# Kernel tuning notes

Measured on AMD Instinct MI355X. Metric: run time of the kernel, lower is better.

The kernel has to match this reference:

```python
import jax, jax.numpy as jnp
import numpy as np

D_MODEL = 2048
NUM_HEADS = 16
KV_HEADS = 4
HEAD_DIM = D_MODEL // NUM_HEADS  # 128
SEQ = 4096
BATCH = 1
ROPE_THETA = 10000.0


def _rope_cache(T, dim, base, dtype):
    inv_freq = 1.0 / (base ** (jnp.arange(0, dim, 2, dtype=jnp.float32) / dim))
    t = jnp.arange(T, dtype=jnp.float32)
    freqs = jnp.outer(t, inv_freq)                      # (T, dim/2)
    emb = jnp.concatenate([freqs, freqs], axis=-1)      # (T, dim)
    return jnp.cos(emb).astype(dtype), jnp.sin(emb).astype(dtype)


def _rotate_half(x):
    d = x.shape[-1] // 2
    return jnp.concatenate([-x[..., d:], x[..., :d]], axis=-1)


def _apply_rope(q, k, cos, sin):
    # q: (B,T,Hq,D), k: (B,T,Hkv,D); cos/sin: (T,D) broadcast over heads
    c = cos[None, :, None, :]
    s = sin[None, :, None, :]
    q = q * c + _rotate_half(q) * s
    k = k * c + _rotate_half(k) * s
    return q, k


def setup_inputs() -> dict:
    key = jax.random.key(0)
    ks = jax.random.split(key, 6)
    sc = 1.0 / np.sqrt(D_MODEL)
    kv_out = KV_HEADS * HEAD_DIM
    return {
        "x": jax.random.normal(ks[0], (BATCH, SEQ, D_MODEL), dtype=jnp.float32),
        "Wq": jax.random.normal(ks[1], (D_MODEL, D_MODEL), dtype=jnp.float32) * sc,
        "Wk": jax.random.normal(ks[2], (D_MODEL, kv_out), dtype=jnp.float32) * sc,
        "Wv": jax.random.normal(ks[3], (D_MODEL, kv_out), dtype=jnp.float32) * sc,
        "Wo": jax.random.normal(ks[4], (D_MODEL, D_MODEL), dtype=jnp.float32) * sc,
        "bo": jax.random.normal(ks[5], (D_MODEL,), dtype=jnp.float32) * 0.01,
    }


def reference(x, Wq, Wk, Wv, Wo, bo):
    B, T, _ = x.shape
    q = (x @ Wq).reshape(B, T, NUM_HEADS, HEAD_DIM)
    k = (x @ Wk).reshape(B, T, KV_HEADS, HEAD_DIM)
    v = (x @ Wv).reshape(B, T, KV_HEADS, HEAD_DIM)

    cos, sin = _rope_cache(T, HEAD_DIM, ROPE_THETA, x.dtype)
    q, k = _apply_rope(q, k, cos, sin)

    reps = NUM_HEADS // KV_HEADS
    k = jnp.repeat(k, reps, axis=2)  # repeat_interleave on head dim
    v = jnp.repeat(v, reps, axis=2)

    # (B,H,T,D)
    q = q.transpose(0, 2, 1, 3)
    k = k.transpose(0, 2, 1, 3)
    v = v.transpose(0, 2, 1, 3)

    scores = jnp.einsum("bhqd,bhkd->bhqk", q, k)
    causal = jnp.triu(jnp.ones((T, T), dtype=bool), k=1)
    scores = jnp.where(causal[None, None], -jnp.inf, scores)
    attn = jax.nn.softmax(scores / jnp.sqrt(jnp.asarray(HEAD_DIM, x.dtype)), axis=-1)

    ctx = jnp.einsum("bhqk,bhkd->bhqd", attn, v)
    ctx = ctx.transpose(0, 2, 1, 3).reshape(B, T, D_MODEL)
    return ctx @ Wo + bo
```

## Files before the change

### kernel.cpp

```cpp
#include <hip/hip_runtime.h>
#include <cstdint>
#include <cstddef>

#define SEQ 4096
#define DM  2048
#define NH  16
#define KVH 4
#define HD  128
#define QSCALE (0.08838834764831845f * 1.4426950408889634f)

typedef short bf16_t;
typedef __attribute__((ext_vector_type(8))) short bf16x8;
typedef __attribute__((ext_vector_type(4))) float f32x4;
typedef __attribute__((ext_vector_type(4))) unsigned uint32x4;

__device__ __forceinline__ bf16_t f2b(float f) {
  unsigned u = __builtin_bit_cast(unsigned, f);
  u += 0x7fffu + ((u >> 16) & 1u);
  return (bf16_t)(u >> 16);
}
__device__ __forceinline__ float b2f(bf16_t s) {
  unsigned u = ((unsigned)(unsigned short)s) << 16;
  return __builtin_bit_cast(float, u);
}
__device__ __forceinline__ unsigned cvtpk(float lo, float hi) {
  unsigned r;
  asm("v_cvt_pk_bf16_f32 %0, %1, %2" : "=v"(r) : "v"(lo), "v"(hi));
  return r;
}

__device__ __forceinline__ void gload_lds16(const void* gsrc, void* ldst) {
  __builtin_amdgcn_global_load_lds(
      (__attribute__((address_space(1))) void*)gsrc,
      (__attribute__((address_space(3))) void*)ldst, 16, 0, 0);
}

__global__ void cast_x_bf16(const float* __restrict__ x, bf16_t* __restrict__ xb, int n4) {
  int i = blockIdx.x * 256 + threadIdx.x;
  if (i >= n4) return;
  float4 v = ((const float4*)x)[i];
  union { bf16_t h[4]; unsigned long long u; } o;
  o.h[0] = f2b(v.x); o.h[1] = f2b(v.y); o.h[2] = f2b(v.z); o.h[3] = f2b(v.w);
  ((unsigned long long*)xb)[i] = o.u;
}

__global__ void transpose_cast_w(const float* __restrict__ W, bf16_t* __restrict__ Wt,
                                 int K, int N) {
  __shared__ float tile[32][33];
  int k0 = blockIdx.y * 32, n0 = blockIdx.x * 32;
  int tx = threadIdx.x, ty = threadIdx.y;
#pragma unroll
  for (int dy = 0; dy < 32; dy += 8)
    tile[ty + dy][tx] = W[(size_t)(k0 + ty + dy) * N + n0 + tx];
  __syncthreads();
#pragma unroll
  for (int dy = 0; dy < 32; dy += 8)
    Wt[(size_t)(n0 + ty + dy) * K + k0 + tx] = f2b(tile[tx][ty + dy]);
}

__global__ void rope_tab(float* __restrict__ ct, float* __restrict__ st) {
  int i = blockIdx.x * 256 + threadIdx.x;
  if (i >= SEQ * 64) return;
  int t = i >> 6, j = i & 63;
  float invf = expf(-(float)j * (9.210340371976184f / 64.0f));
  float ang = (float)t * invf;
  ct[i] = cosf(ang);
  st[i] = sinf(ang);
}

__global__ void rope_apply(bf16_t* __restrict__ Qb, bf16_t* __restrict__ KVb,
                           const float* __restrict__ ct, const float* __restrict__ st) {
  int i = blockIdx.x * 256 + threadIdx.x;
  const int qtot = SEQ * NH * 64;
  const int tot = qtot + SEQ * KVH * 64;
  if (i >= tot) return;
  bf16_t* base; int t, j; float scl;
  if (i < qtot) {
    t = i >> 10; int rem = i & 1023; int hh = rem >> 6; j = rem & 63;
    base = Qb + (size_t)t * DM + hh * HD;
    scl = QSCALE;
  } else {
    int i2 = i - qtot;
    t = i2 >> 8; int rem = i2 & 255; int hh = rem >> 6; j = rem & 63;
    base = KVb + (size_t)t * 1024 + hh * HD;
    scl = 1.0f;
  }
  float c = ct[t * 64 + j], s = st[t * 64 + j];
  float x0 = b2f(base[j]);
  float x1 = b2f(base[j + 64]);
  base[j]      = f2b((x0 * c - x1 * s) * scl);
  base[j + 64] = f2b((x1 * c + x0 * s) * scl);
}

__global__ void transpose_v(const bf16_t* __restrict__ KVb, bf16_t* __restrict__ Vt) {
  __shared__ bf16_t tile[32][33];
  int t0 = blockIdx.y * 32, d0 = blockIdx.x * 32;
  int tx = threadIdx.x, ty = threadIdx.y;
#pragma unroll
  for (int dy = 0; dy < 32; dy += 8)
    tile[ty + dy][tx] = KVb[(size_t)(t0 + ty + dy) * 1024 + 512 + d0 + tx];
  __syncthreads();
  int tt = t0 + tx;
  int j = (tt & ~63) | (tt & 32) | ((tt & 12) << 1) | ((tt & 16) >> 2) | (tt & 3);
#pragma unroll
  for (int dy = 0; dy < 32; dy += 8)
    Vt[(size_t)(d0 + ty + dy) * SEQ + j] = tile[tx][ty + dy];
}

template <int MODE>
__global__ __launch_bounds__(256, MODE == 0 ? 3 : 2)
void gemm_bt(const bf16_t* __restrict__ A, const bf16_t* __restrict__ Bt,
             void* __restrict__ C0out, void* __restrict__ C1out,
             const float* __restrict__ bias, int M, int N, int K) {
  __shared__ __align__(16) bf16_t ldsA[128 * 64];
  __shared__ __align__(16) bf16_t ldsB[128 * 64];
  const int t = threadIdx.x;
  const int w = t >> 6, l = t & 63;
  const int lg = l >> 4, lr = l & 15;
  const int bm = blockIdx.y, bn = blockIdx.x;
  const int wr = (w >> 1) * 64, wc = (w & 1) * 64;

  f32x4 acc[4][4] = {};

  for (int k0 = 0; k0 < K; k0 += 64) {
    __syncthreads();
#pragma unroll
    for (int i = 0; i < 4; ++i) {
      int idx = i * 256 + t;
      int row = idx >> 3;
      int ch  = (idx & 7) ^ (row & 7);
      gload_lds16(A  + (size_t)(bm * 128 + row) * K + k0 + ch * 8, &ldsA[idx * 8]);
      gload_lds16(Bt + (size_t)(bn * 128 + row) * K + k0 + ch * 8, &ldsB[idx * 8]);
    }
    __syncthreads();
#pragma unroll
    for (int kk = 0; kk < 2; ++kk) {
      bf16x8 af[4], bfr[4];
#pragma unroll
      for (int m = 0; m < 4; ++m) {
        int row = wr + m * 16 + lr;
        int ch = (kk * 4 + lg) ^ (row & 7);
        af[m] = *(const bf16x8*)&ldsA[row * 64 + ch * 8];
      }
#pragma unroll
      for (int n = 0; n < 4; ++n) {
        int row = wc + n * 16 + lr;
        int ch = (kk * 4 + lg) ^ (row & 7);
        bfr[n] = *(const bf16x8*)&ldsB[row * 64 + ch * 8];
      }
#pragma unroll
      for (int m = 0; m < 4; ++m)
#pragma unroll
        for (int n = 0; n < 4; ++n)
          acc[m][n] = __builtin_amdgcn_mfma_f32_16x16x32_bf16(af[m], bfr[n], acc[m][n], 0, 0, 0);
    }
  }

  const int row0 = bm * 128 + wr + lg * 4;
  if (MODE == 1) {
    float* C = (float*)C0out;
    const int col0 = bn * 128 + wc + lr;
#pragma unroll
    for (int n = 0; n < 4; ++n) {
      int col = col0 + n * 16;
      float b = bias[col];
#pragma unroll
      for (int m = 0; m < 4; ++m)
#pragma unroll
        for (int r = 0; r < 4; ++r)
          C[(size_t)(row0 + m * 16 + r) * N + col] = acc[m][n][r] + b;
    }
  } else {
    const int colbase = bn * 128 + wc;
    bf16_t* C; int stride, cb;
    if (colbase < 2048) { C = (bf16_t*)C0out; stride = 2048; cb = colbase; }
    else                { C = (bf16_t*)C1out; stride = 1024; cb = colbase - 2048; }
#pragma unroll
    for (int m = 0; m < 4; ++m)
#pragma unroll
      for (int n = 0; n < 4; ++n) {
        int col = cb + n * 16 + lr;
#pragma unroll
        for (int r = 0; r < 4; ++r)
          C[(size_t)(row0 + m * 16 + r) * stride + col] = f2b(acc[m][n][r]);
      }
  }
}

__global__ __launch_bounds__(512, 4)
void attn_fwd(const bf16_t* __restrict__ Qb, const bf16_t* __restrict__ KVb,
              const bf16_t* __restrict__ Vt, bf16_t* __restrict__ ctx) {
  __shared__ __align__(16) bf16_t kt[2][64 * 128];
  __shared__ __align__(16) bf16_t vts[2][128 * 64];

  const int t = threadIdx.x;
  const int w = t >> 6, l = t & 63;
  const int lg = l >> 4, lr = l & 15;
  const int h = blockIdx.y, g = h >> 2;
  const int b = blockIdx.x;
  const int m = w >> 2, wq = w & 3;
  const int qt = m ? 63 - b : b;
  const int qrow0 = qt * 64 + wq * 16;

  bf16x8 qf[4];
#pragma unroll
  for (int kk = 0; kk < 4; ++kk)
    qf[kk] = *(const bf16x8*)&Qb[(size_t)(qrow0 + lr) * DM + h * HD + kk * 32 + lg * 8];

  f32x4 acc[9] = {};
  float m_run = -1e30f;

  bf16x8 ones;
#pragma unroll
  for (int i = 0; i < 8; ++i) ones[i] = (short)0x3F80;

  const bf16_t* ksrc = KVb + g * 128;
  const bf16_t* vsrc = Vt + (size_t)(g * 128) * SEQ;
  auto stage = [&](int buf, int kvt) {
#pragma unroll
    for (int i = 0; i < 2; ++i) {
      int idx = i * 512 + t;
      int row = idx >> 4;
      int ch = (idx & 15) ^ (row & 7);
      gload_lds16(ksrc + (size_t)(kvt * 64 + row) * 1024 + ch * 8, &kt[buf][idx * 8]);
    }
#pragma unroll
    for (int i = 0; i < 2; ++i) {
      int idx = i * 512 + t;
      int row = idx >> 3;
      int ch = (idx & 7) ^ (row & 7);
      gload_lds16(vsrc + (size_t)row * SEQ + kvt * 64 + ch * 8, &vts[buf][idx * 8]);
    }
  };

  const int nkv = 64 - b;
  stage(0, 0);

  for (int kv = 0; kv < nkv; ++kv) {
    const int cur = kv & 1;
    const int kv0 = kv * 64;
    __syncthreads();
    if (kv + 1 < nkv) stage(cur ^ 1, kv + 1);

    if (kv <= qt) {
      f32x4 s[4] = {};
      __builtin_amdgcn_s_setprio(1);
#pragma unroll
      for (int n = 0; n < 4; ++n) {
        int row = n * 16 + lr;
#pragma unroll
        for (int kk = 0; kk < 4; ++kk) {
          int ch = (kk * 4 + lg) ^ (row & 7);
          bf16x8 kf = *(const bf16x8*)&kt[cur][row * 128 + ch * 8];
          s[n] = __builtin_amdgcn_mfma_f32_16x16x32_bf16(kf, qf[kk], s[n], 0, 0, 0);
        }
      }
      __builtin_amdgcn_s_setprio(0);

      const int qrow = qrow0 + lr;
      if (kv == qt) {
#pragma unroll
        for (int n = 0; n < 4; ++n)
#pragma unroll
          for (int r = 0; r < 4; ++r) {
            int key = kv0 + n * 16 + lg * 4 + r;
            if (key > qrow) s[n][r] = -1e30f;
          }
      }

      float pm = s[0][0];
#pragma unroll
      for (int n = 0; n < 4; ++n)
#pragma unroll
        for (int r = 0; r < 4; ++r)
          pm = fmaxf(pm, s[n][r]);
      pm = fmaxf(pm, __shfl_xor(pm, 16, 64));
      pm = fmaxf(pm, __shfl_xor(pm, 32, 64));

      if (__any((int)(pm > m_run + 8.f))) {
        float mn = fmaxf(m_run, pm);
        float a_s = exp2f(m_run - mn);
        m_run = mn;
        float alpha[4];
#pragma unroll
        for (int r = 0; r < 4; ++r)
          alpha[r] = __shfl(a_s, (l & 48) | (lg * 4 + r), 64);
#pragma unroll
        for (int nd = 0; nd < 9; ++nd)
#pragma unroll
          for (int r = 0; r < 4; ++r)
            acc[nd][r] *= alpha[r];
      }

      unsigned u[8];
#pragma unroll
      for (int n = 0; n < 4; ++n) {
        u[2 * n]     = cvtpk(exp2f(s[n][0] - m_run), exp2f(s[n][1] - m_run));
        u[2 * n + 1] = cvtpk(exp2f(s[n][2] - m_run), exp2f(s[n][3] - m_run));
      }
      bf16x8 pf[2];
      pf[0] = __builtin_bit_cast(bf16x8, (uint32x4){u[0], u[1], u[2], u[3]});
      pf[1] = __builtin_bit_cast(bf16x8, (uint32x4){u[4], u[5], u[6], u[7]});

      __builtin_amdgcn_s_setprio(1);
#pragma unroll
      for (int kk2 = 0; kk2 < 2; ++kk2) {
#pragma unroll
        for (int nd = 0; nd < 8; ++nd) {
          int vrow = nd * 16 + lr;
          int vch = (kk2 * 4 + lg) ^ (lr & 7);
          bf16x8 vf = *(const bf16x8*)&vts[cur][vrow * 64 + vch * 8];
          acc[nd] = __builtin_amdgcn_mfma_f32_16x16x32_bf16(pf[kk2], vf, acc[nd], 0, 0, 0);
        }
        acc[8] = __builtin_amdgcn_mfma_f32_16x16x32_bf16(pf[kk2], ones, acc[8], 0, 0, 0);
      }
      __builtin_amdgcn_s_setprio(0);
    }
  }

#pragma unroll
  for (int r = 0; r < 4; ++r) {
    float rl = 1.0f / acc[8][r];
    int qrow = qrow0 + lg * 4 + r;
#pragma unroll
    for (int nd = 0; nd < 8; ++nd) {
      int col = h * HD + nd * 16 + lr;
      ctx[(size_t)qrow * DM + col] = f2b(acc[nd][r] * rl);
    }
  }
}

extern "C" void kernel_launch(void* const* d_in, const int* in_sizes, int n_in,
                              void* d_out, int out_size, void* d_ws, size_t ws_size,
                              hipStream_t stream) {
  const float* x  = (const float*)d_in[0];
  const float* Wq = (const float*)d_in[1];
  const float* Wk = (const float*)d_in[2];
  const float* Wv = (const float*)d_in[3];
  const float* Wo = (const float*)d_in[4];
  const float* bo = (const float*)d_in[5];
  float* out = (float*)d_out;

  char* p = (char*)d_ws;
  bf16_t* xb    = (bf16_t*)p;
  bf16_t* ctx   = xb;
  p += (size_t)SEQ * DM * 2;
  bf16_t* Wqkvt = (bf16_t*)p; p += (size_t)3072 * DM * 2;
  bf16_t* Wot   = (bf16_t*)p; p += (size_t)DM * DM * 2;
  bf16_t* Qb    = (bf16_t*)p; p += (size_t)SEQ * DM * 2;
  bf16_t* KVb   = (bf16_t*)p; p += (size_t)SEQ * 1024 * 2;
  bf16_t* Vt    = (bf16_t*)p; p += (size_t)512 * SEQ * 2;
  float*  ctab  = (float*)p;  p += (size_t)SEQ * 64 * 4;
  float*  stab  = (float*)p;  p += (size_t)SEQ * 64 * 4;

  cast_x_bf16<<<(SEQ * DM / 4 + 255) / 256, 256, 0, stream>>>(x, xb, SEQ * DM / 4);
  transpose_cast_w<<<dim3(DM / 32, DM / 32), dim3(32, 8), 0, stream>>>(Wq, Wqkvt, DM, DM);
  transpose_cast_w<<<dim3(512 / 32, DM / 32), dim3(32, 8), 0, stream>>>(Wk, Wqkvt + (size_t)2048 * DM, DM, 512);
  transpose_cast_w<<<dim3(512 / 32, DM / 32), dim3(32, 8), 0, stream>>>(Wv, Wqkvt + (size_t)2560 * DM, DM, 512);
  transpose_cast_w<<<dim3(DM / 32, DM / 32), dim3(32, 8), 0, stream>>>(Wo, Wot, DM, DM);
  rope_tab<<<(SEQ * 64 + 255) / 256, 256, 0, stream>>>(ctab, stab);

  gemm_bt<0><<<dim3(3072 / 128, SEQ / 128), 256, 0, stream>>>(
      xb, Wqkvt, Qb, KVb, nullptr, SEQ, 3072, DM);

  rope_apply<<<(SEQ * (NH + KVH) * 64 + 255) / 256, 256, 0, stream>>>(Qb, KVb, ctab, stab);
  transpose_v<<<dim3(512 / 32, SEQ / 32), dim3(32, 8), 0, stream>>>(KVb, Vt);

  attn_fwd<<<dim3(32, NH), 512, 0, stream>>>(Qb, KVb, Vt, ctx);

  gemm_bt<1><<<dim3(DM / 128, SEQ / 128), 256, 0, stream>>>(
      ctx, Wot, out, nullptr, bo, SEQ, DM, DM);
}
```

Measured before the change: 268.4 us.

## Software-pipeline attention: overlap previous tile's PV with current QK

The attention loop now issues the P·V MFMAs for the previous KV tile in the same high-priority block as the Q·K MFMAs for the current tile. The softmax exponentials for the current tile then run afterwards, so matrix work can overlap with the exp/convert work instead of waiting on it. V tiles go to a triple-buffered LDS array so the previous tile's V stays valid while the next one is staged. A tail step handles the final tile. This raises LDS use per block and keeps extra P registers live, which may reduce occupancy or add register pressure.

```diff
diff --git a/kernel.cpp b/kernel.cpp
--- a/kernel.cpp
+++ b/kernel.cpp
@@ -191,7 +191,7 @@
 void attn_fwd(const bf16_t* __restrict__ Qb, const bf16_t* __restrict__ KVb,
               const bf16_t* __restrict__ Vt, bf16_t* __restrict__ ctx) {
   __shared__ __align__(16) bf16_t kt[2][64 * 128];
-  __shared__ __align__(16) bf16_t vts[2][128 * 64];
+  __shared__ __align__(16) bf16_t vts[3][128 * 64];
 
   const int t = threadIdx.x;
   const int w = t >> 6, l = t & 63;
@@ -209,6 +209,7 @@
 
   f32x4 acc[9] = {};
   float m_run = -1e30f;
+  bf16x8 pfp[2] = {};
 
   bf16x8 ones;
 #pragma unroll
@@ -216,47 +217,66 @@
 
   const bf16_t* ksrc = KVb + g * 128;
   const bf16_t* vsrc = Vt + (size_t)(g * 128) * SEQ;
-  auto stage = [&](int buf, int kvt) {
+  auto stage = [&](int kbuf, int vbuf, int kvt) {
 #pragma unroll
     for (int i = 0; i < 2; ++i) {
       int idx = i * 512 + t;
       int row = idx >> 4;
       int ch = (idx & 15) ^ (row & 7);
-      gload_lds16(ksrc + (size_t)(kvt * 64 + row) * 1024 + ch * 8, &kt[buf][idx * 8]);
+      gload_lds16(ksrc + (size_t)(kvt * 64 + row) * 1024 + ch * 8, &kt[kbuf][idx * 8]);
     }
 #pragma unroll
     for (int i = 0; i < 2; ++i) {
       int idx = i * 512 + t;
       int row = idx >> 3;
       int ch = (idx & 7) ^ (row & 7);
-      gload_lds16(vsrc + (size_t)row * SEQ + kvt * 64 + ch * 8, &vts[buf][idx * 8]);
+      gload_lds16(vsrc + (size_t)row * SEQ + kvt * 64 + ch * 8, &vts[vbuf][idx * 8]);
     }
   };
 
   const int nkv = 64 - b;
-  stage(0, 0);
+  stage(0, 0, 0);
 
   for (int kv = 0; kv < nkv; ++kv) {
-    const int cur = kv & 1;
+    const int kcur = kv & 1;
+    const int vprev = (kv + 2) % 3;
     const int kv0 = kv * 64;
     __syncthreads();
-    if (kv + 1 < nkv) stage(cur ^ 1, kv + 1);
-
-    if (kv <= qt) {
-      f32x4 s[4] = {};
-      __builtin_amdgcn_s_setprio(1);
+    if (kv + 1 < nkv) stage((kv + 1) & 1, (kv + 1) % 3, kv + 1);
+
+    const bool act  = (kv <= qt);
+    const bool actp = (kv >= 1) && (kv - 1 <= qt);
+
+    f32x4 s[4] = {};
+    __builtin_amdgcn_s_setprio(1);
+    if (act) {
 #pragma unroll
       for (int n = 0; n < 4; ++n) {
         int row = n * 16 + lr;
 #pragma unroll
         for (int kk = 0; kk < 4; ++kk) {
           int ch = (kk * 4 + lg) ^ (row & 7);
-          bf16x8 kf = *(const bf16x8*)&kt[cur][row * 128 + ch * 8];
+          bf16x8 kf = *(const bf16x8*)&kt[kcur][row * 128 + ch * 8];
           s[n] = __builtin_amdgcn_mfma_f32_16x16x32_bf16(kf, qf[kk], s[n], 0, 0, 0);
         }
       }
-      __builtin_amdgcn_s_setprio(0);
-
+    }
+    if (actp) {
+#pragma unroll
+      for (int kk2 = 0; kk2 < 2; ++kk2) {
+#pragma unroll
+        for (int nd = 0; nd < 8; ++nd) {
+          int vrow = nd * 16 + lr;
+          int vch = (kk2 * 4 + lg) ^ (lr & 7);
+          bf16x8 vf = *(const bf16x8*)&vts[vprev][vrow * 64 + vch * 8];
+          acc[nd] = __builtin_amdgcn_mfma_f32_16x16x32_bf16(pfp[kk2], vf, acc[nd], 0, 0, 0);
+        }
+        acc[8] = __builtin_amdgcn_mfma_f32_16x16x32_bf16(pfp[kk2], ones, acc[8], 0, 0, 0);
+      }
+    }
+    __builtin_amdgcn_s_setprio(0);
+
+    if (act) {
       const int qrow = qrow0 + lr;
       if (kv == qt) {
 #pragma unroll
@@ -298,24 +318,26 @@
         u[2 * n]     = cvtpk(exp2f(s[n][0] - m_run), exp2f(s[n][1] - m_run));
         u[2 * n + 1] = cvtpk(exp2f(s[n][2] - m_run), exp2f(s[n][3] - m_run));
       }
-      bf16x8 pf[2];
-      pf[0] = __builtin_bit_cast(bf16x8, (uint32x4){u[0], u[1], u[2], u[3]});
-      pf[1] = __builtin_bit_cast(bf16x8, (uint32x4){u[4], u[5], u[6], u[7]});
-
-      __builtin_amdgcn_s_setprio(1);
-#pragma unroll
-      for (int kk2 = 0; kk2 < 2; ++kk2) {
-#pragma unroll
-        for (int nd = 0; nd < 8; ++nd) {
-          int vrow = nd * 16 + lr;
-          int vch = (kk2 * 4 + lg) ^ (lr & 7);
-          bf16x8 vf = *(const bf16x8*)&vts[cur][vrow * 64 + vch * 8];
-          acc[nd] = __builtin_amdgcn_mfma_f32_16x16x32_bf16(pf[kk2], vf, acc[nd], 0, 0, 0);
-        }
-        acc[8] = __builtin_amdgcn_mfma_f32_16x16x32_bf16(pf[kk2], ones, acc[8], 0, 0, 0);
-      }
-      __builtin_amdgcn_s_setprio(0);
-    }
+      pfp[0] = __builtin_bit_cast(bf16x8, (uint32x4){u[0], u[1], u[2], u[3]});
+      pfp[1] = __builtin_bit_cast(bf16x8, (uint32x4){u[4], u[5], u[6], u[7]});
+    }
+  }
+
+  if (qt == nkv - 1) {
+    const int vlast = (nkv - 1) % 3;
+    __builtin_amdgcn_s_setprio(1);
+#pragma unroll
+    for (int kk2 = 0; kk2 < 2; ++kk2) {
+#pragma unroll
+      for (int nd = 0; nd < 8; ++nd) {
+        int vrow = nd * 16 + lr;
+        int vch = (kk2 * 4 + lg) ^ (lr & 7);
+        bf16x8 vf = *(const bf16x8*)&vts[vlast][vrow * 64 + vch * 8];
+        acc[nd] = __builtin_amdgcn_mfma_f32_16x16x32_bf16(pfp[kk2], vf, acc[nd], 0, 0, 0);
+      }
+      acc[8] = __builtin_amdgcn_mfma_f32_16x16x32_bf16(pfp[kk2], ones, acc[8], 0, 0, 0);
+    }
+    __builtin_amdgcn_s_setprio(0);
   }
 
 #pragma unroll
```

Measured after the change: 283.6 us. 5.7% more time.

## Fuse RoPE into QKV GEMM epilogue and merge prep kernels into one launch

Applied to the files above, without the earlier changes.

Merges the input cast, weight transpose/casts and RoPE table generation into a single prep kernel. The rotary embedding is moved into the QKV GEMM epilogue by permuting the Wq/Wk output rows so each rotary pair sits in adjacent lanes, then rotating with a lane shuffle. This removes the separate rope_apply pass over Q/K and several launches, at the cost of a more complex epilogue with extra table loads.

```diff
diff --git a/kernel.cpp b/kernel.cpp
--- a/kernel.cpp
+++ b/kernel.cpp
@@ -35,61 +35,53 @@
       (__attribute__((address_space(3))) void*)ldst, 16, 0, 0);
 }
 
-__global__ void cast_x_bf16(const float* __restrict__ x, bf16_t* __restrict__ xb, int n4) {
-  int i = blockIdx.x * 256 + threadIdx.x;
-  if (i >= n4) return;
-  float4 v = ((const float4*)x)[i];
-  union { bf16_t h[4]; unsigned long long u; } o;
-  o.h[0] = f2b(v.x); o.h[1] = f2b(v.y); o.h[2] = f2b(v.z); o.h[3] = f2b(v.w);
-  ((unsigned long long*)xb)[i] = o.u;
-}
-
-__global__ void transpose_cast_w(const float* __restrict__ W, bf16_t* __restrict__ Wt,
-                                 int K, int N) {
+__global__ void prep(const float* __restrict__ x, bf16_t* __restrict__ xb,
+                     const float* __restrict__ Wq, const float* __restrict__ Wk,
+                     const float* __restrict__ Wv, const float* __restrict__ Wo,
+                     bf16_t* __restrict__ Wqkvt, bf16_t* __restrict__ Wot,
+                     float* __restrict__ ctT, float* __restrict__ stT) {
   __shared__ float tile[32][33];
-  int k0 = blockIdx.y * 32, n0 = blockIdx.x * 32;
-  int tx = threadIdx.x, ty = threadIdx.y;
+  int bid = blockIdx.x;
+  const int tid = threadIdx.x;
+
+  if (bid < 8192) {
+    int i = bid * 256 + tid;
+    float4 v = ((const float4*)x)[i];
+    union { bf16_t h[4]; unsigned long long u; } o;
+    o.h[0] = f2b(v.x); o.h[1] = f2b(v.y); o.h[2] = f2b(v.z); o.h[3] = f2b(v.w);
+    ((unsigned long long*)xb)[i] = o.u;
+    return;
+  }
+  bid -= 8192;
+  if (bid < 1024) {
+    int i = bid * 256 + tid;
+    int j = i >> 12, t = i & 4095;
+    float invf = expf(-(float)j * (9.210340371976184f / 64.0f));
+    float ang = (float)t * invf;
+    ctT[i] = cosf(ang);
+    stT[i] = sinf(ang);
+    return;
+  }
+  bid -= 1024;
+
+  const float* W; bf16_t* Wt; int N, nx; bool perm;
+  if (bid < 4096)      { W = Wq; Wt = Wqkvt;                          N = 2048; nx = 64; perm = true;  }
+  else if (bid < 5120) { W = Wk; Wt = Wqkvt + (size_t)2048 * DM; bid -= 4096; N = 512; nx = 16; perm = true;  }
+  else if (bid < 6144) { W = Wv; Wt = Wqkvt + (size_t)2560 * DM; bid -= 5120; N = 512; nx = 16; perm = false; }
+  else                 { W = Wo; Wt = Wot;                       bid -= 6144; N = 2048; nx = 64; perm = false; }
+  int bx = bid % nx, by = bid / nx;
+  int k0 = by * 32, n0 = bx * 32;
+  int tx = tid & 31, ty = tid >> 5;
 #pragma unroll
   for (int dy = 0; dy < 32; dy += 8)
     tile[ty + dy][tx] = W[(size_t)(k0 + ty + dy) * N + n0 + tx];
   __syncthreads();
 #pragma unroll
-  for (int dy = 0; dy < 32; dy += 8)
-    Wt[(size_t)(n0 + ty + dy) * K + k0 + tx] = f2b(tile[tx][ty + dy]);
-}
-
-__global__ void rope_tab(float* __restrict__ ct, float* __restrict__ st) {
-  int i = blockIdx.x * 256 + threadIdx.x;
-  if (i >= SEQ * 64) return;
-  int t = i >> 6, j = i & 63;
-  float invf = expf(-(float)j * (9.210340371976184f / 64.0f));
-  float ang = (float)t * invf;
-  ct[i] = cosf(ang);
-  st[i] = sinf(ang);
-}
-
-__global__ void rope_apply(bf16_t* __restrict__ Qb, bf16_t* __restrict__ KVb,
-                           const float* __restrict__ ct, const float* __restrict__ st) {
-  int i = blockIdx.x * 256 + threadIdx.x;
-  const int qtot = SEQ * NH * 64;
-  const int tot = qtot + SEQ * KVH * 64;
-  if (i >= tot) return;
-  bf16_t* base; int t, j; float scl;
-  if (i < qtot) {
-    t = i >> 10; int rem = i & 1023; int hh = rem >> 6; j = rem & 63;
-    base = Qb + (size_t)t * DM + hh * HD;
-    scl = QSCALE;
-  } else {
-    int i2 = i - qtot;
-    t = i2 >> 8; int rem = i2 & 255; int hh = rem >> 6; j = rem & 63;
-    base = KVb + (size_t)t * 1024 + hh * HD;
-    scl = 1.0f;
-  }
-  float c = ct[t * 64 + j], s = st[t * 64 + j];
-  float x0 = b2f(base[j]);
-  float x1 = b2f(base[j + 64]);
-  base[j]      = f2b((x0 * c - x1 * s) * scl);
-  base[j + 64] = f2b((x1 * c + x0 * s) * scl);
+  for (int dy = 0; dy < 32; dy += 8) {
+    int r = n0 + ty + dy;
+    if (perm) r = (r & ~127) | ((r & 63) << 1) | ((r >> 6) & 1);
+    Wt[(size_t)r * DM + k0 + tx] = f2b(tile[tx][ty + dy]);
+  }
 }
 
 __global__ void transpose_v(const bf16_t* __restrict__ KVb, bf16_t* __restrict__ Vt) {
@@ -111,7 +103,8 @@
 __global__ __launch_bounds__(256, MODE == 0 ? 3 : 2)
 void gemm_bt(const bf16_t* __restrict__ A, const bf16_t* __restrict__ Bt,
              void* __restrict__ C0out, void* __restrict__ C1out,
-             const float* __restrict__ bias, int M, int N, int K) {
+             const float* __restrict__ bias, int M, int N, int K,
+             const float* __restrict__ ctT, const float* __restrict__ stT) {
   __shared__ __align__(16) bf16_t ldsA[128 * 64];
   __shared__ __align__(16) bf16_t ldsB[128 * 64];
   const int t = threadIdx.x;
@@ -172,18 +165,44 @@
     }
   } else {
     const int colbase = bn * 128 + wc;
-    bf16_t* C; int stride, cb;
-    if (colbase < 2048) { C = (bf16_t*)C0out; stride = 2048; cb = colbase; }
-    else                { C = (bf16_t*)C1out; stride = 1024; cb = colbase - 2048; }
-#pragma unroll
-    for (int m = 0; m < 4; ++m)
+    if (colbase < 2560) {
+      bf16_t* C; int stride, regbase; float scl;
+      if (colbase < 2048) { C = (bf16_t*)C0out; stride = 2048; regbase = 0;    scl = QSCALE; }
+      else                { C = (bf16_t*)C1out; stride = 1024; regbase = 2048; scl = 1.0f;   }
+      const int odd = lr & 1;
 #pragma unroll
       for (int n = 0; n < 4; ++n) {
-        int col = cb + n * 16 + lr;
-#pragma unroll
-        for (int r = 0; r < 4; ++r)
-          C[(size_t)(row0 + m * 16 + r) * stride + col] = f2b(acc[m][n][r]);
-      }
+        int cpr = colbase + n * 16 + lr;
+        int j = (cpr & 127) >> 1;
+        int colo = (cpr & ~127) - regbase + j + (odd ? 64 : 0);
+#pragma unroll
+        for (int m = 0; m < 4; ++m) {
+          float4 cv = *(const float4*)&ctT[(size_t)j * SEQ + row0 + m * 16];
+          float4 sv = *(const float4*)&stT[(size_t)j * SEQ + row0 + m * 16];
+          float cs[4] = {cv.x, cv.y, cv.z, cv.w};
+          float ss[4] = {sv.x, sv.y, sv.z, sv.w};
+#pragma unroll
+          for (int r = 0; r < 4; ++r) {
+            float a = acc[m][n][r];
+            float b = __shfl_xor(a, 1, 64);
+            float o = odd ? (a * cs[r] + b * ss[r]) : (a * cs[r] - b * ss[r]);
+            C[(size_t)(row0 + m * 16 + r) * stride + colo] = f2b(o * scl);
+          }
+        }
+      }
+    } else {
+      bf16_t* C = (bf16_t*)C1out;
+      const int cb = colbase - 2048;
+#pragma unroll
+      for (int m = 0; m < 4; ++m)
+#pragma unroll
+        for (int n = 0; n < 4; ++n) {
+          int col = cb + n * 16 + lr;
+#pragma unroll
+          for (int r = 0; r < 4; ++r)
+            C[(size_t)(row0 + m * 16 + r) * 1024 + col] = f2b(acc[m][n][r]);
+        }
+    }
   }
 }
 
@@ -350,24 +369,18 @@
   bf16_t* Qb    = (bf16_t*)p; p += (size_t)SEQ * DM * 2;
   bf16_t* KVb   = (bf16_t*)p; p += (size_t)SEQ * 1024 * 2;
   bf16_t* Vt    = (bf16_t*)p; p += (size_t)512 * SEQ * 2;
-  float*  ctab  = (float*)p;  p += (size_t)SEQ * 64 * 4;
-  float*  stab  = (float*)p;  p += (size_t)SEQ * 64 * 4;
-
-  cast_x_bf16<<<(SEQ * DM / 4 + 255) / 256, 256, 0, stream>>>(x, xb, SEQ * DM / 4);
-  transpose_cast_w<<<dim3(DM / 32, DM / 32), dim3(32, 8), 0, stream>>>(Wq, Wqkvt, DM, DM);
-  transpose_cast_w<<<dim3(512 / 32, DM / 32), dim3(32, 8), 0, stream>>>(Wk, Wqkvt + (size_t)2048 * DM, DM, 512);
-  transpose_cast_w<<<dim3(512 / 32, DM / 32), dim3(32, 8), 0, stream>>>(Wv, Wqkvt + (size_t)2560 * DM, DM, 512);
-  transpose_cast_w<<<dim3(DM / 32, DM / 32), dim3(32, 8), 0, stream>>>(Wo, Wot, DM, DM);
-  rope_tab<<<(SEQ * 64 + 255) / 256, 256, 0, stream>>>(ctab, stab);
+  float*  ctT   = (float*)p;  p += (size_t)64 * SEQ * 4;
+  float*  stT   = (float*)p;  p += (size_t)64 * SEQ * 4;
+
+  prep<<<19456, 256, 0, stream>>>(x, xb, Wq, Wk, Wv, Wo, Wqkvt, Wot, ctT, stT);
 
   gemm_bt<0><<<dim3(3072 / 128, SEQ / 128), 256, 0, stream>>>(
-      xb, Wqkvt, Qb, KVb, nullptr, SEQ, 3072, DM);
-
-  rope_apply<<<(SEQ * (NH + KVH) * 64 + 255) / 256, 256, 0, stream>>>(Qb, KVb, ctab, stab);
+      xb, Wqkvt, Qb, KVb, nullptr, SEQ, 3072, DM, ctT, stT);
+
   transpose_v<<<dim3(512 / 32, SEQ / 32), dim3(32, 8), 0, stream>>>(KVb, Vt);
 
   attn_fwd<<<dim3(32, NH), 512, 0, stream>>>(Qb, KVb, Vt, ctx);
 
   gemm_bt<1><<<dim3(DM / 128, SEQ / 128), 256, 0, stream>>>(
-      ctx, Wot, out, nullptr, bo, SEQ, DM, DM);
-}
+      ctx, Wot, out, nullptr, bo, SEQ, DM, DM, nullptr, nullptr);
+}
```

Result: faster. 255.0 us (-5.0%).
